# Kernel tuning notes

Hardware: AMD Instinct MI355X
Metric: run time of the kernel (lower is better)

The kernel has to match this reference:

```python
import jax, jax.numpy as jnp
import numpy as np

DISTANCE_W = 1.0
ANGLE_W = 1.0
EPS = 1e-12  # matches F.normalize eps


def setup_inputs() -> dict:
    key = jax.random.key(0)
    k1, k2 = jax.random.split(key)
    student_emb = jax.random.normal(k1, (1024, 512), dtype=jnp.float32)
    teacher_emb = jax.random.normal(k2, (1024, 512), dtype=jnp.float32)
    return {"student_emb": student_emb, "teacher_emb": teacher_emb}


def _pairwise_similarity(emb):
    # F.normalize(emb, dim=1) then emb @ emb.T -> [N, N] cosine similarity
    norm = jnp.maximum(jnp.linalg.norm(emb, axis=1, keepdims=True), EPS)
    en = emb / norm
    return en @ en.T


def _angle_similarity(emb):
    # ||e_i - e_j||^2 for all pairs, computed via the GEMM expansion
    # (same math as the N x N x D broadcast in the original, no O(N^2 D) tensor)
    sq = jnp.sum(emb * emb, axis=1)  # [N]
    gram = emb @ emb.T               # [N, N]
    return sq[:, None] + sq[None, :] - 2.0 * gram


def reference(student_emb, teacher_emb):
    loss_dist = jnp.mean((_pairwise_similarity(student_emb) - _pairwise_similarity(teacher_emb)) ** 2)
    loss_angle = jnp.mean((_angle_similarity(student_emb) - _angle_similarity(teacher_emb)) ** 2)
    return DISTANCE_W * loss_dist + ANGLE_W * loss_angle
```

## Files before the change

### kernel.cpp

```cpp
#include <hip/hip_runtime.h>

typedef short short8 __attribute__((ext_vector_type(8)));
typedef float f32x4 __attribute__((ext_vector_type(4)));
typedef unsigned short ushort;

#define DD 512


__device__ __forceinline__ short to_bf16(float f) {
    unsigned int u = __float_as_uint(f);
    u += 0x7FFFu + ((u >> 16) & 1u);
    return (short)(u >> 16);
}

__device__ __forceinline__ short8 pack8(float4 a, float4 b) {
    short8 r;
    r[0] = to_bf16(a.x); r[1] = to_bf16(a.y); r[2] = to_bf16(a.z); r[3] = to_bf16(a.w);
    r[4] = to_bf16(b.x); r[5] = to_bf16(b.y); r[6] = to_bf16(b.z); r[7] = to_bf16(b.w);
    return r;
}

__device__ __forceinline__ float dot4(float4 v) {
    return v.x*v.x + v.y*v.y + v.z*v.z + v.w*v.w;
}

__global__ __launch_bounds__(256) void convert_kernel(const float* __restrict__ S,
                                                      const float* __restrict__ T,
                                                      ushort* __restrict__ bf,
                                                      float* __restrict__ sqarr,
                                                      float* __restrict__ accw) {
    const int t    = threadIdx.x;
    const int lane = t & 63;
    const int row  = blockIdx.x * 4 + (t >> 6);
    const float* src = (row < 1024) ? (S + (size_t)row * DD)
                                    : (T + (size_t)(row - 1024) * DD);
    float4 v0 = ((const float4*)src)[lane * 2];
    float4 v1 = ((const float4*)src)[lane * 2 + 1];
    *(short8*)(bf + (size_t)row * DD + lane * 8) = pack8(v0, v1);
    float s = dot4(v0) + dot4(v1);
    #pragma unroll
    for (int off = 32; off > 0; off >>= 1) s += __shfl_down(s, off);
    if (lane == 0) {
        sqarr[row]        = s;
        sqarr[2048 + row] = 1.0f / fmaxf(sqrtf(s), 1e-12f);
    }
    if (blockIdx.x == 0 && t < 17) ((unsigned int*)(accw))[t] = 0u;
}

__global__ __launch_bounds__(256, 2) void rkd_tile_kernel(const ushort* __restrict__ bf,
                                                          const float* __restrict__ sqarr,
                                                          float* __restrict__ accw,
                                                          float* __restrict__ out) {
    __shared__ ushort tiles[2][12288];
    __shared__ float wsum[4];

    const int t = threadIdx.x;
    const int I = (blockIdx.x >> 5) * 64;
    const int J = (blockIdx.x & 31) * 32;
    const int w = t >> 6;
    const int L = t & 63;
    const int m = L & 15;
    const int quad = L >> 4;
    const int arow = w * 16 + m;

    const ushort* bS = bf;
    const ushort* bT = bf + (size_t)1024 * DD;

    const int lrow  = L >> 3;
    const int lchk  = (L & 7) ^ lrow;
    const int lgoff = lrow * DD + lchk * 8;

    const ushort* gtab[6];
    int loff[6];
    #pragma unroll
    for (int j = 0; j < 6; ++j) {
        const int q = w * 6 + j;
        const ushort* gmat; int gbase, lo;
        if (q < 8)       { gmat = bS; gbase = I; lo = 0     + q * 512; }
        else if (q < 16) { gmat = bT; gbase = I; lo = 4096  + (q - 8) * 512; }
        else if (q < 20) { gmat = bS; gbase = J; lo = 8192  + (q - 16) * 512; }
        else             { gmat = bT; gbase = J; lo = 10240 + (q - 20) * 512; }
        const int rbase = (lo & 4095) >> 6;
        (void)rbase;
        gtab[j] = gmat + (size_t)gbase * DD + (size_t)((lo * 8) & 0)  + lgoff
                  + (size_t)(((q < 8) ? q : (q < 16) ? (q - 8) : (q < 20) ? (q - 16) : (q - 20)) * 8) * DD;
        loff[j] = lo;
    }

    const int j0 = J + m, j1 = J + 16 + m;
    const float js0 = sqarr[j0],        jt0 = sqarr[1024 + j0];
    const float rjs0 = sqarr[2048 + j0], rjt0 = sqarr[3072 + j0];
    const float js1 = sqarr[j1],        jt1 = sqarr[1024 + j1];
    const float rjs1 = sqarr[2048 + j1], rjt1 = sqarr[3072 + j1];
    const int ib = I + w * 16 + quad * 4;
    float isv[4], itv[4], risv[4], ritv[4];
    #pragma unroll
    for (int reg = 0; reg < 4; ++reg) {
        isv[reg]  = sqarr[ib + reg];        itv[reg]  = sqarr[1024 + ib + reg];
        risv[reg] = sqarr[2048 + ib + reg]; ritv[reg] = sqarr[3072 + ib + reg];
    }

    f32x4 aS0 = {0,0,0,0}, aS1 = {0,0,0,0};
    f32x4 aT0 = {0,0,0,0}, aT1 = {0,0,0,0};

    #pragma unroll
    for (int j = 0; j < 6; ++j)
        __builtin_amdgcn_global_load_lds(
            (const __attribute__((address_space(1))) void*)(gtab[j]),
            (__attribute__((address_space(3))) void*)(&tiles[0][0] + loff[j]), 16, 0, 0);

    for (int i = 0; i < 8; ++i) {
        __syncthreads();
        if (i < 7) {
            const int nb = (i + 1) & 1;
            const int k0 = (i + 1) * 64;
            #pragma unroll
            for (int j = 0; j < 6; ++j)
                __builtin_amdgcn_global_load_lds(
                    (const __attribute__((address_space(1))) void*)(gtab[j] + k0),
                    (__attribute__((address_space(3))) void*)(&tiles[nb][0] + loff[j]), 16, 0, 0);
        }
        const ushort* base = &tiles[i & 1][0];
        #pragma unroll
        for (int ks = 0; ks < 2; ++ks) {
            const int cs = ((ks * 4 + quad) ^ (m & 7)) * 8;
            short8 af_s = *(const short8*)(base + arow * 64 + cs);
            short8 af_t = *(const short8*)(base + 4096 + arow * 64 + cs);
            short8 b_s0 = *(const short8*)(base + 8192 + m * 64 + cs);
            short8 b_s1 = *(const short8*)(base + 8192 + (16 + m) * 64 + cs);
            short8 b_t0 = *(const short8*)(base + 10240 + m * 64 + cs);
            short8 b_t1 = *(const short8*)(base + 10240 + (16 + m) * 64 + cs);
            aS0 = __builtin_amdgcn_mfma_f32_16x16x32_bf16(af_s, b_s0, aS0, 0, 0, 0);
            aS1 = __builtin_amdgcn_mfma_f32_16x16x32_bf16(af_s, b_s1, aS1, 0, 0, 0);
            aT0 = __builtin_amdgcn_mfma_f32_16x16x32_bf16(af_t, b_t0, aT0, 0, 0, 0);
            aT1 = __builtin_amdgcn_mfma_f32_16x16x32_bf16(af_t, b_t1, aT1, 0, 0, 0);
        }
    }

    float local = 0.0f;
    #pragma unroll
    for (int reg = 0; reg < 4; ++reg) {
        float is = isv[reg], it = itv[reg], ris = risv[reg], rit = ritv[reg];

        float gs0 = aS0[reg], gt0 = aT0[reg];
        float d1 = gs0 * ris * rjs0 - gt0 * rit * rjt0;
        float d2 = (is + js0 - 2.0f * gs0) - (it + jt0 - 2.0f * gt0);
        local += d1 * d1 + d2 * d2;

        float gs1 = aS1[reg], gt1 = aT1[reg];
        float e1 = gs1 * ris * rjs1 - gt1 * rit * rjt1;
        float e2 = (is + js1 - 2.0f * gs1) - (it + jt1 - 2.0f * gt1);
        local += e1 * e1 + e2 * e2;
    }

    #pragma unroll
    for (int off = 32; off > 0; off >>= 1) local += __shfl_down(local, off);
    if (L == 0) wsum[w] = local;
    __syncthreads();

    if (t == 0) {
        float blk = wsum[0] + wsum[1] + wsum[2] + wsum[3];
        atomicAdd(&accw[blockIdx.x & 15], blk);
        __threadfence();
        unsigned int old = atomicAdd((unsigned int*)(accw + 16), 1u);
        if (old == 511u) {
            __threadfence();
            float tot = 0.0f;
            #pragma unroll
            for (int s2 = 0; s2 < 16; ++s2)
                tot += __hip_atomic_load(&accw[s2], __ATOMIC_RELAXED, __HIP_MEMORY_SCOPE_AGENT);
            out[0] = tot * (1.0f / 1048576.0f);
        }
    }
}

extern "C" void kernel_launch(void* const* d_in, const int* in_sizes, int n_in,
                              void* d_out, int out_size, void* d_ws, size_t ws_size,
                              hipStream_t stream) {
    const float* S = (const float*)d_in[0];
    const float* T = (const float*)d_in[1];
    ushort* bf   = (ushort*)d_ws;
    float* sqarr = (float*)((char*)d_ws + 2 * 1024 * 1024);
    float* accw  = sqarr + 4096;
    float* out   = (float*)d_out;

    convert_kernel<<<512, 256, 0, stream>>>(S, T, bf, sqarr, accw);
    rkd_tile_kernel<<<512, 256, 0, stream>>>(bf, sqarr, accw, out);
}
```

Before: 75.93 us.

## Use 64x64 output tiles with 32x32x16 MFMA and LDS-staged row statistics

Each block now covers a 64x64 tile of the pairwise matrices instead of 64x32, halving the grid to 256 blocks. Each wave computes a 32x32 sub-tile with the 32x32x16 bf16 MFMA instead of several 16x16x32 ones. Per-row norms and inverse norms are staged in shared memory so the epilogue can index them. This cuts redundant global-to-LDS loading of the J-side tiles, in exchange for more LDS per block and a grid that is too small to fill every CU on the device.

```diff
diff --git a/kernel.cpp b/kernel.cpp
--- a/kernel.cpp
+++ b/kernel.cpp
@@ -1,7 +1,7 @@
 #include <hip/hip_runtime.h>
 
 typedef short short8 __attribute__((ext_vector_type(8)));
-typedef float f32x4 __attribute__((ext_vector_type(4)));
+typedef float f32x16 __attribute__((ext_vector_type(16)));
 typedef unsigned short ushort;
 
 #define DD 512
@@ -47,64 +47,58 @@
     if (blockIdx.x == 0 && t < 17) ((unsigned int*)(accw))[t] = 0u;
 }
 
-__global__ __launch_bounds__(256, 2) void rkd_tile_kernel(const ushort* __restrict__ bf,
-                                                          const float* __restrict__ sqarr,
-                                                          float* __restrict__ accw,
-                                                          float* __restrict__ out) {
-    __shared__ ushort tiles[2][12288];
+__global__ __launch_bounds__(256) void rkd_tile_kernel(const ushort* __restrict__ bf,
+                                                       const float* __restrict__ sqarr,
+                                                       float* __restrict__ accw,
+                                                       float* __restrict__ out) {
+    __shared__ ushort tiles[2][16384];
+    __shared__ float statI[4][64];
+    __shared__ float statJ[4][64];
     __shared__ float wsum[4];
 
     const int t = threadIdx.x;
-    const int I = (blockIdx.x >> 5) * 64;
-    const int J = (blockIdx.x & 31) * 32;
+    const int I = (blockIdx.x >> 4) * 64;
+    const int J = (blockIdx.x & 15) * 64;
     const int w = t >> 6;
     const int L = t & 63;
-    const int m = L & 15;
-    const int quad = L >> 4;
-    const int arow = w * 16 + m;
+    const int c = L & 31;
+    const int h = L >> 5;
+    const int rowsel = (w & 1) * 32;
+    const int colsel = (w >> 1) * 32;
 
     const ushort* bS = bf;
     const ushort* bT = bf + (size_t)1024 * DD;
+
+    {
+        const int a = t >> 6, r = t & 63;
+        const int so = a * 1024;
+        statI[a][r] = sqarr[so + I + r];
+        statJ[a][r] = sqarr[so + J + r];
+    }
 
     const int lrow  = L >> 3;
     const int lchk  = (L & 7) ^ lrow;
     const int lgoff = lrow * DD + lchk * 8;
 
-    const ushort* gtab[6];
-    int loff[6];
+    const ushort* gtab[8];
+    int loff[8];
     #pragma unroll
-    for (int j = 0; j < 6; ++j) {
-        const int q = w * 6 + j;
-        const ushort* gmat; int gbase, lo;
-        if (q < 8)       { gmat = bS; gbase = I; lo = 0     + q * 512; }
-        else if (q < 16) { gmat = bT; gbase = I; lo = 4096  + (q - 8) * 512; }
-        else if (q < 20) { gmat = bS; gbase = J; lo = 8192  + (q - 16) * 512; }
-        else             { gmat = bT; gbase = J; lo = 10240 + (q - 20) * 512; }
-        const int rbase = (lo & 4095) >> 6;
-        (void)rbase;
-        gtab[j] = gmat + (size_t)gbase * DD + (size_t)((lo * 8) & 0)  + lgoff
-                  + (size_t)(((q < 8) ? q : (q < 16) ? (q - 8) : (q < 20) ? (q - 16) : (q - 20)) * 8) * DD;
-        loff[j] = lo;
+    for (int j = 0; j < 8; ++j) {
+        const int q   = w * 8 + j;
+        const int ts  = q >> 3;
+        const int sub = q & 7;
+        const ushort* gmat = (ts == 0 || ts == 2) ? bS : bT;
+        const int gbase = (ts < 2) ? I : J;
+        gtab[j] = gmat + (size_t)(gbase + sub * 8) * DD + lgoff;
+        loff[j] = ts * 4096 + sub * 512;
     }
 
-    const int j0 = J + m, j1 = J + 16 + m;
-    const float js0 = sqarr[j0],        jt0 = sqarr[1024 + j0];
-    const float rjs0 = sqarr[2048 + j0], rjt0 = sqarr[3072 + j0];
-    const float js1 = sqarr[j1],        jt1 = sqarr[1024 + j1];
-    const float rjs1 = sqarr[2048 + j1], rjt1 = sqarr[3072 + j1];
-    const int ib = I + w * 16 + quad * 4;
-    float isv[4], itv[4], risv[4], ritv[4];
+    f32x16 accS, accT;
     #pragma unroll
-    for (int reg = 0; reg < 4; ++reg) {
-        isv[reg]  = sqarr[ib + reg];        itv[reg]  = sqarr[1024 + ib + reg];
-        risv[reg] = sqarr[2048 + ib + reg]; ritv[reg] = sqarr[3072 + ib + reg];
-    }
-
-    f32x4 aS0 = {0,0,0,0}, aS1 = {0,0,0,0};
-    f32x4 aT0 = {0,0,0,0}, aT1 = {0,0,0,0};
+    for (int i2 = 0; i2 < 16; ++i2) { accS[i2] = 0.0f; accT[i2] = 0.0f; }
 
     #pragma unroll
-    for (int j = 0; j < 6; ++j)
+    for (int j = 0; j < 8; ++j)
         __builtin_amdgcn_global_load_lds(
             (const __attribute__((address_space(1))) void*)(gtab[j]),
             (__attribute__((address_space(3))) void*)(&tiles[0][0] + loff[j]), 16, 0, 0);
@@ -112,45 +106,41 @@
     for (int i = 0; i < 8; ++i) {
         __syncthreads();
         if (i < 7) {
-            const int nb = (i + 1) & 1;
             const int k0 = (i + 1) * 64;
+            ushort* nb = &tiles[(i + 1) & 1][0];
             #pragma unroll
-            for (int j = 0; j < 6; ++j)
+            for (int j = 0; j < 8; ++j)
                 __builtin_amdgcn_global_load_lds(
                     (const __attribute__((address_space(1))) void*)(gtab[j] + k0),
-                    (__attribute__((address_space(3))) void*)(&tiles[nb][0] + loff[j]), 16, 0, 0);
+                    (__attribute__((address_space(3))) void*)(nb + loff[j]), 16, 0, 0);
         }
         const ushort* base = &tiles[i & 1][0];
         #pragma unroll
-        for (int ks = 0; ks < 2; ++ks) {
-            const int cs = ((ks * 4 + quad) ^ (m & 7)) * 8;
-            short8 af_s = *(const short8*)(base + arow * 64 + cs);
-            short8 af_t = *(const short8*)(base + 4096 + arow * 64 + cs);
-            short8 b_s0 = *(const short8*)(base + 8192 + m * 64 + cs);
-            short8 b_s1 = *(const short8*)(base + 8192 + (16 + m) * 64 + cs);
-            short8 b_t0 = *(const short8*)(base + 10240 + m * 64 + cs);
-            short8 b_t1 = *(const short8*)(base + 10240 + (16 + m) * 64 + cs);
-            aS0 = __builtin_amdgcn_mfma_f32_16x16x32_bf16(af_s, b_s0, aS0, 0, 0, 0);
-            aS1 = __builtin_amdgcn_mfma_f32_16x16x32_bf16(af_s, b_s1, aS1, 0, 0, 0);
-            aT0 = __builtin_amdgcn_mfma_f32_16x16x32_bf16(af_t, b_t0, aT0, 0, 0, 0);
-            aT1 = __builtin_amdgcn_mfma_f32_16x16x32_bf16(af_t, b_t1, aT1, 0, 0, 0);
+        for (int step = 0; step < 4; ++step) {
+            const int us = ((step * 2 + h) ^ (c & 7)) * 8;
+            short8 afS = *(const short8*)(base + (rowsel + c) * 64 + us);
+            short8 afT = *(const short8*)(base + 4096 + (rowsel + c) * 64 + us);
+            short8 bfS = *(const short8*)(base + 8192 + (colsel + c) * 64 + us);
+            short8 bfT = *(const short8*)(base + 12288 + (colsel + c) * 64 + us);
+            accS = __builtin_amdgcn_mfma_f32_32x32x16_bf16(afS, bfS, accS, 0, 0, 0);
+            accT = __builtin_amdgcn_mfma_f32_32x32x16_bf16(afT, bfT, accT, 0, 0, 0);
         }
     }
 
+    const int colg = colsel + c;
+    const float js  = statJ[0][colg], jt  = statJ[1][colg];
+    const float rjs = statJ[2][colg], rjt = statJ[3][colg];
+
     float local = 0.0f;
     #pragma unroll
-    for (int reg = 0; reg < 4; ++reg) {
-        float is = isv[reg], it = itv[reg], ris = risv[reg], rit = ritv[reg];
-
-        float gs0 = aS0[reg], gt0 = aT0[reg];
-        float d1 = gs0 * ris * rjs0 - gt0 * rit * rjt0;
-        float d2 = (is + js0 - 2.0f * gs0) - (it + jt0 - 2.0f * gt0);
+    for (int reg = 0; reg < 16; ++reg) {
+        const int rowg = rowsel + (reg & 3) + 8 * (reg >> 2) + 4 * h;
+        float is  = statI[0][rowg], it  = statI[1][rowg];
+        float ris = statI[2][rowg], rit = statI[3][rowg];
+        float gs = accS[reg], gt = accT[reg];
+        float d1 = gs * ris * rjs - gt * rit * rjt;
+        float d2 = (is + js - 2.0f * gs) - (it + jt - 2.0f * gt);
         local += d1 * d1 + d2 * d2;
-
-        float gs1 = aS1[reg], gt1 = aT1[reg];
-        float e1 = gs1 * ris * rjs1 - gt1 * rit * rjt1;
-        float e2 = (is + js1 - 2.0f * gs1) - (it + jt1 - 2.0f * gt1);
-        local += e1 * e1 + e2 * e2;
     }
 
     #pragma unroll
@@ -163,7 +153,7 @@
         atomicAdd(&accw[blockIdx.x & 15], blk);
         __threadfence();
         unsigned int old = atomicAdd((unsigned int*)(accw + 16), 1u);
-        if (old == 511u) {
+        if (old == 255u) {
             __threadfence();
             float tot = 0.0f;
             #pragma unroll
@@ -185,5 +175,5 @@
     float* out   = (float*)d_out;
 
     convert_kernel<<<512, 256, 0, stream>>>(S, T, bf, sqarr, accw);
-    rkd_tile_kernel<<<512, 256, 0, stream>>>(bf, sqarr, accw, out);
+    rkd_tile_kernel<<<256, 256, 0, stream>>>(bf, sqarr, accw, out);
 }
```

New measurement: 72.72 us. 4.2% less time.
